# Kernel optimization log

Measured on AMD Instinct MI355X. Metric: run time of the kernel, lower is better.

Reference implementation:

```python
import math
import jax, jax.numpy as jnp
import numpy as np

L, B, E, NDIM = 4096, 4, 1024, 16


def setup_inputs() -> dict:
    key = jax.random.key(0)
    ks = jax.random.split(key, 6)
    x = jax.random.normal(ks[0], (L, B, E), dtype=jnp.float32)
    alpha = jax.random.normal(ks[1], (2 * E, NDIM, 1), dtype=jnp.float32) * 0.2
    delta = jax.random.normal(ks[2], (2 * E, NDIM, 1), dtype=jnp.float32) * 0.2
    # beta init: N(0, 0.02) + alternating +-1 along ndim
    val = np.ones((NDIM, 1), dtype=np.float32)
    val[1::2] = -1.0
    beta = jax.random.normal(ks[3], (2 * E, NDIM, 1), dtype=jnp.float32) * 0.02 + jnp.asarray(val)
    gamma = jax.random.normal(ks[4], (2 * E, NDIM), dtype=jnp.float32)
    omega = jax.random.normal(ks[5], (E,), dtype=jnp.float32)
    return {"x": x, "alpha": alpha, "delta": delta, "beta": beta, "gamma": gamma, "omega": omega}


def reference(x, alpha, delta, beta, gamma, omega):
    seq_len, bsz, embed_dim = x.shape
    ndim = alpha.shape[1]
    scale = math.sqrt(1.0 / ndim)

    residual = x * omega  # (L, B, E)
    xc = jnp.transpose(x, (1, 2, 0))  # (B, E, L)

    a = jax.nn.sigmoid(alpha)
    d = jax.nn.sigmoid(delta)
    q = 1.0 - a * d          # (2E, ndim, 1)
    p = a * beta             # (2E, ndim, 1)

    t = jnp.arange(seq_len, dtype=x.dtype)          # (L,)
    vander = t[None, None, :] * jnp.log(q)          # (2E, ndim, L)
    kernel = p * jnp.exp(vander)                    # (2E, ndim, L)
    k = jnp.einsum('dnl,dn->dl', kernel, gamma * scale)  # (2E, L)

    fft_len = 2 * seq_len  # seq_len + kernel_size (truncation=None)
    k1, k2 = k[:embed_dim], k[embed_dim:]
    # bidirectional + shift: causal part padded right, flipped anti-causal padded left
    kb = jnp.pad(k1, ((0, 0), (0, seq_len))) + jnp.pad(k2[:, ::-1], ((0, 0), (seq_len, 0)))  # (E, 2L)

    k_f = jnp.fft.rfft(kb, n=fft_len)   # (E, L+1) complex
    x_f = jnp.fft.rfft(xc, n=fft_len)   # (B, E, L+1) complex
    out = jnp.fft.irfft(x_f * k_f, n=fft_len)[..., :seq_len]  # (B, E, L)
    out = out.astype(x.dtype)

    return jax.nn.silu(jnp.transpose(out, (2, 0, 1)) + residual)  # (L, B, E)
```

## Files before the change

kernel.cpp:

```cpp
#include <hip/hip_runtime.h>
#include <hip/hip_bf16.h>
#include <math.h>

#define L_  4096
#define B_  4
#define E_  1024
#define ND  16
#define CK  64
#define NC  (L_/CK)
#define BE  (B_*E_)
#define COLS (BE*ND)

#define OFF_Q   0
#define OFF_W   (2*E_*ND)
#define OFF_QC  (2*2*E_*ND)
#define OFF_FS  (3*2*E_*ND)
#define OFF_GR  (OFF_FS + (size_t)NC*COLS)

__device__ __forceinline__ float sigm(float x){ return 1.0f/(1.0f+__expf(-x)); }

__global__ void k_params(const float* __restrict__ al,
                         const float* __restrict__ de,
                         const float* __restrict__ be,
                         const float* __restrict__ ga,
                         float* __restrict__ ws){
    int i = blockIdx.x*256 + threadIdx.x;
    float a = sigm(al[i]);
    float d = sigm(de[i]);
    float q = 1.0f - a*d;
    float w = a*be[i]*ga[i]*0.25f;
    float qc = q;
    #pragma unroll
    for(int k=0;k<6;k++) qc *= qc;
    ws[OFF_Q+i]=q; ws[OFF_W+i]=w; ws[OFF_QC+i]=qc;
}

__global__ __launch_bounds__(256) void k_summ(const float* __restrict__ x,
                                              float* __restrict__ ws){
    int bid = blockIdx.x;
    int c  = bid >> 4;
    int b  = (bid >> 2) & 3;
    int eg = bid & 3;
    int e  = eg*256 + threadIdx.x;
    const float* Q = ws + OFF_Q;
    float qf[ND], qb[ND], F[ND], G[ND];
    #pragma unroll
    for(int n=0;n<ND;n++){
        qf[n]=Q[e*ND+n]; qb[n]=Q[(E_+e)*ND+n]; F[n]=0.f; G[n]=0.f;
    }
    const float* xp = x + (size_t)(c*CK)*BE + b*E_ + e;
    #pragma unroll 4
    for(int i=0;i<CK;i++){
        float xa = xp[(size_t)i*BE];
        float xb = xp[(size_t)(CK-1-i)*BE];
        #pragma unroll
        for(int n=0;n<ND;n++){
            F[n]=fmaf(qf[n],F[n],xa);
            G[n]=fmaf(qb[n],G[n],xb);
        }
    }
    int col = (b*E_+e)*ND;
    float* Fp = ws + OFF_FS + (size_t)c*COLS + col;
    float* Gp = ws + OFF_GR + (size_t)c*COLS + col;
    #pragma unroll
    for(int n=0;n<ND;n++){ Fp[n]=F[n]; Gp[n]=G[n]; }
}

__global__ __launch_bounds__(256) void k_scan(float* __restrict__ ws){
    int t = blockIdx.x*256 + threadIdx.x;
    int bwd = (t >= COLS);
    int col = bwd ? (t - COLS) : t;
    int e = (col >> 4) & (E_-1);
    int n = col & (ND-1);
    if(!bwd){
        float qc = ws[OFF_QC + e*ND + n];
        float s = 0.f;
        float* Fb = ws + OFF_FS;
        #pragma unroll 4
        for(int c=1;c<NC;c++){
            float f = Fb[(size_t)(c-1)*COLS + col];
            s = fmaf(qc, s, f);
            Fb[(size_t)(c-1)*COLS + col] = s;
        }
    } else {
        float qc = ws[OFF_QC + (E_+e)*ND + n];
        float r = 0.f;
        float* Gb = ws + OFF_GR;
        #pragma unroll 4
        for(int c=NC-1;c>=0;c--){
            float g = Gb[(size_t)c*COLS + col];
            r = fmaf(qc, r, g);
            Gb[(size_t)c*COLS + col] = r;
        }
    }
}

__global__ __launch_bounds__(256) void k_out(const float* __restrict__ x,
                                             const float* __restrict__ om,
                                             const float* __restrict__ ws,
                                             float* __restrict__ out){
    __shared__ float part[CK*256];
    int bid = blockIdx.x;
    int c  = bid >> 4;
    int b  = (bid >> 2) & 3;
    int eg = bid & 3;
    int e  = eg*256 + threadIdx.x;
    const float* Q = ws + OFF_Q;
    const float* W = ws + OFF_W;
    float q1[ND], w1[ND], q2[ND], w2[ND], st[ND];
    #pragma unroll
    for(int n=0;n<ND;n++){
        q1[n]=Q[e*ND+n];       w1[n]=W[e*ND+n];
        q2[n]=Q[(E_+e)*ND+n];  w2[n]=W[(E_+e)*ND+n];
    }
    float omg = om[e];
    int col = (b*E_+e)*ND;

    if(c==0){
        #pragma unroll
        for(int n=0;n<ND;n++) st[n]=0.f;
    } else {
        const float* Sp = ws + OFF_FS + (size_t)(c-1)*COLS + col;
        #pragma unroll
        for(int n=0;n<ND;n++) st[n]=Sp[n];
    }
    const float* xp = x + (size_t)(c*CK)*BE + b*E_ + e;
    #pragma unroll 4
    for(int i=0;i<CK;i++){
        float xv = xp[(size_t)i*BE];
        float acc = xv*omg;
        #pragma unroll
        for(int n=0;n<ND;n++){
            st[n]=fmaf(q1[n],st[n],xv);
            acc  =fmaf(w1[n],st[n],acc);
        }
        part[i*256+threadIdx.x] = acc;
    }

    float rt[ND];
    if(c==NC-1){
        #pragma unroll
        for(int n=0;n<ND;n++) rt[n]=0.f;
    } else {
        const float* Rp = ws + OFF_GR + (size_t)(c+1)*COLS + col;
        #pragma unroll
        for(int n=0;n<ND;n++) rt[n]=Rp[n];
    }
    float* op = out + (size_t)(c*CK)*BE + b*E_ + e;
    #pragma unroll 4
    for(int i=CK-1;i>=0;i--){
        float acc = part[i*256+threadIdx.x];
        #pragma unroll
        for(int n=0;n<ND;n++) acc = fmaf(w2[n], rt[n], acc);
        float z = acc;
        float o = z / (1.0f + __expf(-z));
        op[(size_t)i*BE] = o;
        float xv = xp[(size_t)i*BE];
        #pragma unroll
        for(int n=0;n<ND;n++) rt[n]=fmaf(q2[n],rt[n],xv);
    }
}

extern "C" void kernel_launch(void* const* d_in, const int* in_sizes, int n_in,
                              void* d_out, int out_size, void* d_ws, size_t ws_size,
                              hipStream_t stream) {
    const float* x  = (const float*)d_in[0];
    const float* al = (const float*)d_in[1];
    const float* de = (const float*)d_in[2];
    const float* be = (const float*)d_in[3];
    const float* ga = (const float*)d_in[4];
    const float* om = (const float*)d_in[5];
    float* ws = (float*)d_ws;
    float* out = (float*)d_out;

    k_params<<<dim3((2*E_*ND)/256), dim3(256), 0, stream>>>(al, de, be, ga, ws);
    k_summ  <<<dim3(NC*B_*(E_/256)), dim3(256), 0, stream>>>(x, ws);
    k_scan  <<<dim3((2*COLS)/256), dim3(256), 0, stream>>>(ws);
    k_out   <<<dim3(NC*B_*(E_/256)), dim3(256), 0, stream>>>(x, om, ws, out);
}
```

Measured before the change: 210.9 us.

## Store k_out partials as fp16, preload scan chunks, tweak unroll and occupancy

k_out's shared-memory buffer of forward-pass partial sums now holds fp16 instead of fp32. This halves LDS use so more blocks fit per CU, and the launch bounds now request 5 blocks per SM. k_scan loads all chunk values into registers before running the sequential recurrence, which puts the global loads ahead of the dependent FMA chain. k_summ's unroll factor goes from 4 to 8. The fp16 partials lose precision on values that include the x*omega residual and the causal sum, which may break the accuracy tolerance.

```diff
diff --git a/kernel.cpp b/kernel.cpp
--- a/kernel.cpp
+++ b/kernel.cpp
@@ -1,5 +1,6 @@
 #include <hip/hip_runtime.h>
 #include <hip/hip_bf16.h>
+#include <hip/hip_fp16.h>
 #include <math.h>
 
 #define L_  4096
@@ -49,7 +50,7 @@
         qf[n]=Q[e*ND+n]; qb[n]=Q[(E_+e)*ND+n]; F[n]=0.f; G[n]=0.f;
     }
     const float* xp = x + (size_t)(c*CK)*BE + b*E_ + e;
-    #pragma unroll 4
+    #pragma unroll 8
     for(int i=0;i<CK;i++){
         float xa = xp[(size_t)i*BE];
         float xb = xp[(size_t)(CK-1-i)*BE];
@@ -74,32 +75,36 @@
     int n = col & (ND-1);
     if(!bwd){
         float qc = ws[OFF_QC + e*ND + n];
+        float* Fb = ws + OFF_FS + col;
+        float v[NC-1];
+        #pragma unroll
+        for(int c=0;c<NC-1;c++) v[c] = Fb[(size_t)c*COLS];
         float s = 0.f;
-        float* Fb = ws + OFF_FS;
-        #pragma unroll 4
-        for(int c=1;c<NC;c++){
-            float f = Fb[(size_t)(c-1)*COLS + col];
-            s = fmaf(qc, s, f);
-            Fb[(size_t)(c-1)*COLS + col] = s;
+        #pragma unroll
+        for(int c=0;c<NC-1;c++){
+            s = fmaf(qc, s, v[c]);
+            Fb[(size_t)c*COLS] = s;
         }
     } else {
         float qc = ws[OFF_QC + (E_+e)*ND + n];
+        float* Gb = ws + OFF_GR + col;
+        float v[NC];
+        #pragma unroll
+        for(int c=0;c<NC;c++) v[c] = Gb[(size_t)c*COLS];
         float r = 0.f;
-        float* Gb = ws + OFF_GR;
-        #pragma unroll 4
+        #pragma unroll
         for(int c=NC-1;c>=0;c--){
-            float g = Gb[(size_t)c*COLS + col];
-            r = fmaf(qc, r, g);
-            Gb[(size_t)c*COLS + col] = r;
+            r = fmaf(qc, r, v[c]);
+            Gb[(size_t)c*COLS] = r;
         }
     }
 }
 
-__global__ __launch_bounds__(256) void k_out(const float* __restrict__ x,
-                                             const float* __restrict__ om,
-                                             const float* __restrict__ ws,
-                                             float* __restrict__ out){
-    __shared__ float part[CK*256];
+__global__ __launch_bounds__(256, 5) void k_out(const float* __restrict__ x,
+                                                const float* __restrict__ om,
+                                                const float* __restrict__ ws,
+                                                float* __restrict__ out){
+    __shared__ __half part[CK*256];
     int bid = blockIdx.x;
     int c  = bid >> 4;
     int b  = (bid >> 2) & 3;
@@ -134,7 +139,7 @@
             st[n]=fmaf(q1[n],st[n],xv);
             acc  =fmaf(w1[n],st[n],acc);
         }
-        part[i*256+threadIdx.x] = acc;
+        part[i*256+threadIdx.x] = __float2half_rn(acc);
     }
 
     float rt[ND];
@@ -149,7 +154,7 @@
     float* op = out + (size_t)(c*CK)*BE + b*E_ + e;
     #pragma unroll 4
     for(int i=CK-1;i>=0;i--){
-        float acc = part[i*256+threadIdx.x];
+        float acc = __half2float(part[i*256+threadIdx.x]);
         #pragma unroll
         for(int n=0;n<ND;n++) acc = fmaf(w2[n], rt[n], acc);
         float z = acc;
```

Measured after the change: 200.7 us. 1.05x faster.
